# Kernel tuning notes

Hardware: AMD Instinct MI355X
Metric: run time of the kernel (lower is better)

The kernel has to match this reference:

```python
import jax, jax.numpy as jnp
import numpy as np

N_NODES = 100000
N_EDGES = 1600000
IN_F = 128
OUT_F = 32
NHEAD = 4
ALPHA = 0.2  # leaky relu negative slope


def setup_inputs() -> dict:
    key = jax.random.key(0)
    k1, k2, k3, k4, k5 = jax.random.split(key, 5)
    x = jax.random.normal(k1, (N_NODES, IN_F), dtype=jnp.float32)
    edge_index = jax.random.randint(k2, (2, N_EDGES), 0, N_NODES, dtype=jnp.int32)
    # glorot-ish init as in reset_parameters
    stdv_w = np.sqrt(6.0 / (IN_F + OUT_F * NHEAD))
    W = jax.random.uniform(k3, (IN_F, OUT_F * NHEAD), minval=-stdv_w, maxval=stdv_w, dtype=jnp.float32)
    stdv_a = np.sqrt(6.0 / (NHEAD + OUT_F))
    a_l = jax.random.uniform(k4, (1, NHEAD, OUT_F), minval=-stdv_a, maxval=stdv_a, dtype=jnp.float32)
    a_r = jax.random.uniform(k5, (1, NHEAD, OUT_F), minval=-stdv_a, maxval=stdv_a, dtype=jnp.float32)
    return {"x": x, "edge_index": edge_index, "W": W, "a_l": a_l, "a_r": a_r}


def reference(x, edge_index, W, a_l, a_r):
    N = x.shape[0]
    # h: [N, nhead, out]
    h = jnp.matmul(x, W).reshape(N, NHEAD, OUT_F)
    h = jnp.nan_to_num(h)
    row, col = edge_index[0], edge_index[1]
    # per-node attention halves: [N, nhead]
    al = (a_l * h).sum(axis=-1)
    ar = (a_r * h).sum(axis=-1)
    # per-edge raw scores: [E, nhead]
    e = jax.nn.leaky_relu(al[row] + ar[col], negative_slope=ALPHA)
    # segment softmax over incoming edges of each destination node (row)
    m = jax.ops.segment_max(e, row, num_segments=N)           # [N, nhead]
    e_exp = jnp.exp(e - m[row])                               # [E, nhead]
    s = jax.ops.segment_sum(e_exp, row, num_segments=N)       # [N, nhead]
    att = e_exp / s[row]                                      # [E, nhead]
    # spmm aggregation per head: out[i] = sum_{(i,j) in E} att_ij * h[j]
    msg = att[:, :, None] * h[col]                            # [E, nhead, out]
    out = jax.ops.segment_sum(msg, row, num_segments=N)       # [N, nhead, out]
    return out.reshape(N, NHEAD * OUT_F)
```

## Files before the change

### kernel.cpp

```cpp
#include <hip/hip_runtime.h>
#include <hip/hip_bf16.h>
#include <string.h>

#define NN 100000
#define NE 1600000
#define INF_ 128
#define OC 128
#define NH 4
#define ALPHA 0.2f
#define LDA 272

#define BSH 7
#define BINW 128
#define NBIN ((NN + BINW - 1) / BINW)
#define CAPB 2560
#define SCOLS_CAP (CAPB + 3 * BINW / 2 + 16)
#define EPT 16
#define EPB (256 * EPT)
#define NPB1 ((NE + EPB - 1) / EPB)

typedef __bf16 bf16x8 __attribute__((ext_vector_type(8)));
typedef float f32x4 __attribute__((ext_vector_type(4)));
typedef float f32x2 __attribute__((ext_vector_type(2)));

__device__ __forceinline__ float lrelu(float x) {
    return x > 0.0f ? x : ALPHA * x;
}
__device__ __forceinline__ unsigned short f2bf(float f) {
    __hip_bfloat16 b = __float2bfloat16(f);
    unsigned short u; memcpy(&u, &b, 2); return u;
}
__device__ __forceinline__ int sel4(const int4 v, int j) {
    const int lo = (j & 1) ? v.y : v.x;
    const int hi = (j & 1) ? v.w : v.z;
    return (j & 2) ? hi : lo;
}

__global__ __launch_bounds__(256) void k_pre(
    const float* __restrict__ W, const float* __restrict__ a_l,
    const float* __restrict__ a_r, __hip_bfloat16* __restrict__ Wt,
    int* __restrict__ bincur) {
    const int t = threadIdx.x;
    const int b = blockIdx.x;
    if (b < 64) {
        const int i = b * 256 + t;
        const int co = i >> 7, ko = i & 127;
        Wt[i] = __float2bfloat16(W[ko * OC + co]);
    } else {
        const int i = (b - 64) * 256 + t;
        const int cp = i >> 7, k = i & 127;
        float v = 0.f;
        if (cp < 8) {
            const int hd = cp & 3;
            const float* av = (cp < 4) ? a_l : a_r;
#pragma unroll 8
            for (int j = 0; j < 32; ++j)
                v += W[k * OC + hd * 32 + j] * av[hd * 32 + j];
        }
        Wt[(128 + cp) * 128 + k] = __float2bfloat16(v);
    }
    if (b == 0)
        for (int i = t; i < NBIN; i += 256) bincur[i] = i * CAPB;
}

__global__ __launch_bounds__(256) void k_gp1(
    const float* __restrict__ x, const __hip_bfloat16* __restrict__ Wt,
    __hip_bfloat16* __restrict__ hb, float* __restrict__ al, float* __restrict__ ar,
    const int* __restrict__ row, const int* __restrict__ col,
    int* __restrict__ bincur, unsigned* __restrict__ tmp) {
    __shared__ __align__(16) char smem[144 * LDA];
    const int tid = threadIdx.x;
    const int m5 = blockIdx.x % 5;

    if (m5 != 4) {
        char* sB = smem;
        const int gb = (blockIdx.x / 5) * 4 + m5;
        const int rowBase = gb * 64;

        for (int i4 = tid; i4 < 144 * 16; i4 += 256) {
            const int c = i4 >> 4, k4 = i4 & 15;
            *(uint4*)(sB + c * LDA + k4 * 16) =
                *(const uint4*)((const char*)Wt + (size_t)c * 256 + k4 * 16);
        }
        __syncthreads();

        const int lane = tid & 63;
        const int w = tid >> 6;
        const int arow = w * 16 + (lane & 15);
        const int grow = rowBase + arow;
        const int growc = (grow < NN) ? grow : (NN - 1);
        const int koff8 = (lane >> 4) * 8;
        const int koff = (lane >> 4) * 16;

        f32x4 acc[9];
#pragma unroll
        for (int n = 0; n < 9; ++n) acc[n] = (f32x4){0.f, 0.f, 0.f, 0.f};

#pragma unroll
        for (int kk = 0; kk < 4; ++kk) {
            const float* xp = x + (size_t)growc * INF_ + kk * 32 + koff8;
            const float4 f0 = *(const float4*)xp;
            const float4 f1 = *(const float4*)(xp + 4);
            union { bf16x8 v; unsigned short u[8]; } au;
            au.u[0] = f2bf(f0.x); au.u[1] = f2bf(f0.y);
            au.u[2] = f2bf(f0.z); au.u[3] = f2bf(f0.w);
            au.u[4] = f2bf(f1.x); au.u[5] = f2bf(f1.y);
            au.u[6] = f2bf(f1.z); au.u[7] = f2bf(f1.w);
#pragma unroll
            for (int n = 0; n < 9; ++n) {
                const int brow = n * 16 + (lane & 15);
                const bf16x8 b = *(const bf16x8*)(sB + brow * LDA + kk * 64 + koff);
                acc[n] = __builtin_amdgcn_mfma_f32_16x16x32_bf16(au.v, b, acc[n], 0, 0, 0);
            }
        }

        const int rbase = rowBase + w * 16 + (lane >> 4) * 4;
#pragma unroll
        for (int n = 0; n < 8; ++n) {
            const int cc = n * 16 + (lane & 15);
#pragma unroll
            for (int r = 0; r < 4; ++r) {
                const int rw = rbase + r;
                if (rw < NN) hb[(size_t)rw * OC + cc] = __float2bfloat16(acc[n][r]);
            }
        }
        const int cp = lane & 15;
        if (cp < 8) {
            const int hd = cp & 3;
            float* dst = (cp < 4) ? al : ar;
#pragma unroll
            for (int r = 0; r < 4; ++r) {
                const int rw = rbase + r;
                if (rw < NN) dst[rw * NH + hd] = acc[8][r];
            }
        }
    } else {
        int* h     = (int*)smem;
        int* gbase = h + NBIN;
        int* lcur  = gbase + NBIN;
        const int pb = blockIdx.x / 5;
        const int t = tid;
        for (int i = t; i < NBIN; i += 256) { h[i] = 0; lcur[i] = 0; }
        __syncthreads();

        const int e0 = pb * EPB + t * EPT;
        int r[EPT], c[EPT];
        if (e0 + EPT <= NE) {
#pragma unroll
            for (int q = 0; q < EPT / 4; ++q) {
                const int4 rv = *(const int4*)&row[e0 + q * 4];
                const int4 cv = *(const int4*)&col[e0 + q * 4];
                r[q*4+0] = rv.x; r[q*4+1] = rv.y; r[q*4+2] = rv.z; r[q*4+3] = rv.w;
                c[q*4+0] = cv.x; c[q*4+1] = cv.y; c[q*4+2] = cv.z; c[q*4+3] = cv.w;
            }
        } else {
#pragma unroll
            for (int i = 0; i < EPT; ++i) {
                const int e = e0 + i;
                r[i] = (e < NE) ? row[e] : -1;
                c[i] = (e < NE) ? col[e] : 0;
            }
        }
#pragma unroll
        for (int i = 0; i < EPT; ++i)
            if (r[i] >= 0) atomicAdd(&h[r[i] >> BSH], 1);
        __syncthreads();
        for (int i = t; i < NBIN; i += 256)
            if (h[i]) gbase[i] = atomicAdd(&bincur[i], h[i]);
        __syncthreads();
#pragma unroll
        for (int i = 0; i < EPT; ++i) {
            if (r[i] < 0) continue;
            const int b = r[i] >> BSH;
            const int pos = atomicAdd(&lcur[b], 1);
            tmp[gbase[b] + pos] =
                ((unsigned)(r[i] & (BINW - 1)) << 17) | (unsigned)c[i];
        }
    }
}

__global__ __launch_bounds__(512) void k_p2agg(
    const unsigned* __restrict__ tmp, const int* __restrict__ bincur,
    const float* __restrict__ al, const float* __restrict__ ar,
    const __hip_bfloat16* __restrict__ hb, float* __restrict__ out) {
    __shared__ __align__(16) unsigned stage[CAPB];
    __shared__ __align__(16) int scols[SCOLS_CAP];
    __shared__ int h[BINW], st[BINW], cur[BINW], ts[BINW];
    const int b = blockIdx.x;
    const int t = threadIdx.x;
    const int gs = b * CAPB;
    const int cnt = bincur[b] - gs;

    if (t < BINW) h[t] = 0;
    __syncthreads();
    for (int j = t; j < cnt; j += 512) {
        const unsigned p = tmp[gs + j];
        stage[j] = p;
        atomicAdd(&h[p >> 17], 1);
    }
    __syncthreads();
    if (t < BINW) ts[t] = (h[t] + 3) & ~3;
    __syncthreads();
    for (int o = 1; o < BINW; o <<= 1) {
        const int add = (t >= o && t < BINW) ? ts[t - o] : 0;
        __syncthreads();
        if (t < BINW) ts[t] += add;
        __syncthreads();
    }
    if (t < BINW) {
        const int s = ts[t] - ((h[t] + 3) & ~3);
        st[t] = s;
        cur[t] = s;
    }
    __syncthreads();
    for (int j = t; j < cnt; j += 512) {
        const unsigned p = stage[j];
        const int pos = atomicAdd(&cur[p >> 17], 1);
        scols[pos] = (int)(p & 0x1FFFFu);
    }
    __syncthreads();

    const int w = t >> 6;
    const int lane = t & 63;
    const int g = lane >> 4;
    const int sl = lane & 15;
    const int hsel = sl >> 2;
    const int je = sl >> 2;
    const int sh = sl & 3;
    const int sbase = lane & 48;
    const char* hrow = (const char*)hb + sl * 16;

    for (int rnd = 0; rnd < BINW / 32; ++rnd) {
        const int ln = rnd * 32 + w * 4 + g;
        const int node = b * BINW + ln;
        if (node >= NN) continue;
        const int start = st[ln];
        const int deg = h[ln];
        const float al_sh = al[node * NH + sh];

        f32x2 a0 = {0.f, 0.f}, a1 = {0.f, 0.f}, a2 = {0.f, 0.f}, a3 = {0.f, 0.f};
        float ssum = 0.f;

        int4 cA = *(const int4*)(scols + start);
        int4 cB = *(const int4*)(scols + start + 4);

        for (int kk = 0; kk < deg; kk += 8) {
            const int rem = deg - kk;
            const int4 cA2 = *(const int4*)(scols + start + kk + 8);
            const int4 cB2 = *(const int4*)(scols + start + kk + 12);

            float wvA = 0.f, wvB = 0.f;
            if (je < rem) {
                const int c = sel4(cA, je);
                wvA = __expf(lrelu(al_sh + ar[c * NH + sh]));
            }
            if (je + 4 < rem) {
                const int c = sel4(cB, je);
                wvB = __expf(lrelu(al_sh + ar[c * NH + sh]));
            }

            int c_[8] = {cA.x, cA.y, cA.z, cA.w, cB.x, cB.y, cB.z, cB.w};
#pragma unroll
            for (int j = 0; j < 8; ++j)
                if (j >= rem) c_[j] = 0;

#pragma unroll
            for (int j = 0; j < 8; ++j) {
                const float wj = __shfl(j < 4 ? wvA : wvB, sbase + (j & 3) * 4 + hsel);
                const uint4 v = *(const uint4*)(hrow + (size_t)c_[j] * 256);
                a0 += wj * (f32x2){__uint_as_float(v.x << 16), __uint_as_float(v.x & 0xffff0000u)};
                a1 += wj * (f32x2){__uint_as_float(v.y << 16), __uint_as_float(v.y & 0xffff0000u)};
                a2 += wj * (f32x2){__uint_as_float(v.z << 16), __uint_as_float(v.z & 0xffff0000u)};
                a3 += wj * (f32x2){__uint_as_float(v.w << 16), __uint_as_float(v.w & 0xffff0000u)};
                ssum += wj;
            }
            cA = cA2; cB = cB2;
        }

        const float inv = (ssum > 0.f) ? 1.0f / ssum : 0.f;
        float4 o0, o1;
        o0.x = a0.x * inv; o0.y = a0.y * inv; o0.z = a1.x * inv; o0.w = a1.y * inv;
        o1.x = a2.x * inv; o1.y = a2.y * inv; o1.z = a3.x * inv; o1.w = a3.y * inv;
        float* dst = out + (size_t)node * OC + sl * 8;
        *(float4*)dst = o0;
        *(float4*)(dst + 4) = o1;
    }
}

extern "C" void kernel_launch(void* const* d_in, const int* in_sizes, int n_in,
                              void* d_out, int out_size, void* d_ws, size_t ws_size,
                              hipStream_t stream) {
    const float* x    = (const float*)d_in[0];
    const int*   ei   = (const int*)d_in[1];
    const float* W    = (const float*)d_in[2];
    const float* a_l  = (const float*)d_in[3];
    const float* a_r  = (const float*)d_in[4];
    float* out = (float*)d_out;

    const int* row = ei;
    const int* col = ei + NE;

    char* ws = (char*)d_ws;
    __hip_bfloat16* hb = (__hip_bfloat16*)ws;   ws += (size_t)NN * OC * 2;
    __hip_bfloat16* Wt = (__hip_bfloat16*)ws;   ws += (size_t)144 * 128 * 2;
    float*    al      = (float*)ws;             ws += (size_t)NN * NH * 4;
    float*    ar      = (float*)ws;             ws += (size_t)NN * NH * 4;
    unsigned* tmp     = (unsigned*)ws;          ws += (size_t)NBIN * CAPB * 4;
    int*      bincur  = (int*)ws;               ws += (size_t)NBIN * 4;

    k_pre<<<72, 256, 0, stream>>>(W, a_l, a_r, Wt, bincur);
    k_gp1<<<1955, 256, 0, stream>>>(x, Wt, hb, al, ar, row, col, bincur, tmp);
    k_p2agg<<<NBIN, 512, 0, stream>>>(tmp, bincur, al, ar, hb, out);
}
```

Before: 123.5 us.

## Split h features into two head-pair halves and route aggregation blocks per XCD

Stores the bf16 projected features as two separate 64-column arrays, one per pair of heads. The aggregation grid doubles so that each bin is handled by two blocks, one per head pair. Block indices are mapped so that blocks reading the same half land on the same XCD group, which shrinks each XCD's gathered working set and should improve L2 hit rates. In exchange, the shared-memory binning and sort work is duplicated across both blocks of each bin.

```diff
diff --git a/kernel.cpp b/kernel.cpp
--- a/kernel.cpp
+++ b/kernel.cpp
@@ -13,6 +13,7 @@
 #define BSH 7
 #define BINW 128
 #define NBIN ((NN + BINW - 1) / BINW)
+#define NBIN4 784
 #define CAPB 2560
 #define SCOLS_CAP (CAPB + 3 * BINW / 2 + 16)
 #define EPT 16
@@ -65,7 +66,8 @@
 
 __global__ __launch_bounds__(256) void k_gp1(
     const float* __restrict__ x, const __hip_bfloat16* __restrict__ Wt,
-    __hip_bfloat16* __restrict__ hb, float* __restrict__ al, float* __restrict__ ar,
+    __hip_bfloat16* __restrict__ hb0, __hip_bfloat16* __restrict__ hb1,
+    float* __restrict__ al, float* __restrict__ ar,
     const int* __restrict__ row, const int* __restrict__ col,
     int* __restrict__ bincur, unsigned* __restrict__ tmp) {
     __shared__ __align__(16) char smem[144 * LDA];
@@ -117,11 +119,12 @@
         const int rbase = rowBase + w * 16 + (lane >> 4) * 4;
 #pragma unroll
         for (int n = 0; n < 8; ++n) {
-            const int cc = n * 16 + (lane & 15);
+            const int cc = (n * 16 + (lane & 15)) & 63;
+            __hip_bfloat16* hbn = (n < 4) ? hb0 : hb1;
 #pragma unroll
             for (int r = 0; r < 4; ++r) {
                 const int rw = rbase + r;
-                if (rw < NN) hb[(size_t)rw * OC + cc] = __float2bfloat16(acc[n][r]);
+                if (rw < NN) hbn[(size_t)rw * 64 + cc] = __float2bfloat16(acc[n][r]);
             }
         }
         const int cp = lane & 15;
@@ -182,11 +185,15 @@
 __global__ __launch_bounds__(512) void k_p2agg(
     const unsigned* __restrict__ tmp, const int* __restrict__ bincur,
     const float* __restrict__ al, const float* __restrict__ ar,
-    const __hip_bfloat16* __restrict__ hb, float* __restrict__ out) {
+    const __hip_bfloat16* __restrict__ hb0, const __hip_bfloat16* __restrict__ hb1,
+    float* __restrict__ out) {
     __shared__ __align__(16) unsigned stage[CAPB];
     __shared__ __align__(16) int scols[SCOLS_CAP];
     __shared__ int h[BINW], st[BINW], cur[BINW], ts[BINW];
-    const int b = blockIdx.x;
+    const int xcd = blockIdx.x & 7;
+    const int hp  = xcd >> 2;
+    const int b   = ((blockIdx.x >> 3) << 2) + (xcd & 3);
+    if (b >= NBIN) return;
     const int t = threadIdx.x;
     const int gs = b * CAPB;
     const int cnt = bincur[b] - gs;
@@ -222,16 +229,17 @@
 
     const int w = t >> 6;
     const int lane = t & 63;
-    const int g = lane >> 4;
-    const int sl = lane & 15;
-    const int hsel = sl >> 2;
-    const int je = sl >> 2;
-    const int sh = sl & 3;
-    const int sbase = lane & 48;
-    const char* hrow = (const char*)hb + sl * 16;
-
-    for (int rnd = 0; rnd < BINW / 32; ++rnd) {
-        const int ln = rnd * 32 + w * 4 + g;
+    const int g = lane >> 3;
+    const int sl = lane & 7;
+    const int hh = sl >> 2;
+    const int je = sl >> 1;
+    const int sh = hp * 2 + (sl & 1);
+    const int sbase = lane & 56;
+    const __hip_bfloat16* hbh = hp ? hb1 : hb0;
+    const char* hrow = (const char*)hbh + sl * 16;
+
+    for (int rnd = 0; rnd < BINW / 64; ++rnd) {
+        const int ln = rnd * 64 + w * 8 + g;
         const int node = b * BINW + ln;
         if (node >= NN) continue;
         const int start = st[ln];
@@ -266,8 +274,8 @@
 
 #pragma unroll
             for (int j = 0; j < 8; ++j) {
-                const float wj = __shfl(j < 4 ? wvA : wvB, sbase + (j & 3) * 4 + hsel);
-                const uint4 v = *(const uint4*)(hrow + (size_t)c_[j] * 256);
+                const float wj = __shfl(j < 4 ? wvA : wvB, sbase + (j & 3) * 2 + hh);
+                const uint4 v = *(const uint4*)(hrow + (size_t)c_[j] * 128);
                 a0 += wj * (f32x2){__uint_as_float(v.x << 16), __uint_as_float(v.x & 0xffff0000u)};
                 a1 += wj * (f32x2){__uint_as_float(v.y << 16), __uint_as_float(v.y & 0xffff0000u)};
                 a2 += wj * (f32x2){__uint_as_float(v.z << 16), __uint_as_float(v.z & 0xffff0000u)};
@@ -281,7 +289,7 @@
         float4 o0, o1;
         o0.x = a0.x * inv; o0.y = a0.y * inv; o0.z = a1.x * inv; o0.w = a1.y * inv;
         o1.x = a2.x * inv; o1.y = a2.y * inv; o1.z = a3.x * inv; o1.w = a3.y * inv;
-        float* dst = out + (size_t)node * OC + sl * 8;
+        float* dst = out + (size_t)node * OC + hp * 64 + sl * 8;
         *(float4*)dst = o0;
         *(float4*)(dst + 4) = o1;
     }
@@ -301,7 +309,8 @@
     const int* col = ei + NE;
 
     char* ws = (char*)d_ws;
-    __hip_bfloat16* hb = (__hip_bfloat16*)ws;   ws += (size_t)NN * OC * 2;
+    __hip_bfloat16* hb0 = (__hip_bfloat16*)ws;  ws += (size_t)NN * 64 * 2;
+    __hip_bfloat16* hb1 = (__hip_bfloat16*)ws;  ws += (size_t)NN * 64 * 2;
     __hip_bfloat16* Wt = (__hip_bfloat16*)ws;   ws += (size_t)144 * 128 * 2;
     float*    al      = (float*)ws;             ws += (size_t)NN * NH * 4;
     float*    ar      = (float*)ws;             ws += (size_t)NN * NH * 4;
@@ -309,6 +318,6 @@
     int*      bincur  = (int*)ws;               ws += (size_t)NBIN * 4;
 
     k_pre<<<72, 256, 0, stream>>>(W, a_l, a_r, Wt, bincur);
-    k_gp1<<<1955, 256, 0, stream>>>(x, Wt, hb, al, ar, row, col, bincur, tmp);
-    k_p2agg<<<NBIN, 512, 0, stream>>>(tmp, bincur, al, ar, hb, out);
-}
+    k_gp1<<<1955, 256, 0, stream>>>(x, Wt, hb0, hb1, al, ar, row, col, bincur, tmp);
+    k_p2agg<<<2 * NBIN4, 512, 0, stream>>>(tmp, bincur, al, ar, hb0, hb1, out);
+}
```

After: 126.4 us. 1.02x slower.
